# Optimization experiments

Hardware: AMD Instinct MI355X
Metric: run time of the kernel (lower is better)

## Reference

```python
import jax, jax.numpy as jnp
import numpy as np

Q, C, D, H, K, B, T = 10000, 200, 64, 64, 4, 512, 200
MAX_DISC = 10.0


def setup_inputs() -> dict:
    key = jax.random.key(0)
    ks = jax.random.split(key, 24)

    def p(k, shape, s=0.05):
        return jax.random.normal(k, shape, jnp.float32) * s

    mid_qd = (D + C) // 2   # 132
    mid_la = (H + C) // 2   # 132
    mid_dc = (D + 1) // 2   # 32
    inp = {
        'E_q': p(ks[0], (Q + 1, D)),
        'E_c': p(ks[1], (C + 1, D)),
        'E_it': p(ks[2], (101, D)),
        'E_ut': p(ks[3], (101, D)),
        'E_nh': p(ks[4], (101, D)),
        'W_fuse': p(ks[5], (D, 3 * D)), 'b_fuse': jnp.zeros((D,), jnp.float32),
        'W_ih': p(ks[6], (3 * H, 5 * D)), 'b_ih': jnp.zeros((3 * H,), jnp.float32),
        'W_hh': p(ks[7], (3 * H, H)), 'b_hh': jnp.zeros((3 * H,), jnp.float32),
        'qd_W1': p(ks[8], (mid_qd, D)), 'qd_b1': jnp.zeros((mid_qd,), jnp.float32),
        'qd_W2': p(ks[9], (C, mid_qd)), 'qd_b2': jnp.zeros((C,), jnp.float32),
        'la_W1': p(ks[10], (mid_la, H)), 'la_b1': jnp.zeros((mid_la,), jnp.float32),
        'la_W2': p(ks[11], (C, mid_la)), 'la_b2': jnp.zeros((C,), jnp.float32),
        'dc_W1': p(ks[12], (mid_dc, D)), 'dc_b1': jnp.zeros((mid_dc,), jnp.float32),
        'dc_W2': p(ks[13], (1, mid_dc)), 'dc_b2': jnp.zeros((1,), jnp.float32),
    }
    inp['question_seq'] = jax.random.randint(ks[14], (B, T), 0, Q + 1, jnp.int32)
    inp['correct_seq'] = jax.random.randint(ks[15], (B, T), 0, 2, jnp.int32)
    inp['interval_time_seq'] = jax.random.randint(ks[16], (B, T), 0, 101, jnp.int32)
    inp['use_time_seq'] = jax.random.randint(ks[17], (B, T), 0, 101, jnp.int32)
    inp['num_hint_seq'] = jax.random.randint(ks[18], (B, T), 0, 101, jnp.int32)
    inp['num_attempt_seq'] = jax.random.randint(ks[19], (B, T), 0, 101, jnp.int32)
    # per-question concept lists + padding mask (first nc entries valid)
    q2c = jax.random.randint(ks[20], (Q + 1, K), 0, C, jnp.int32)
    nc = jax.random.randint(ks[21], (Q + 1,), 1, K + 1, jnp.int32)
    mask = (jnp.arange(K, dtype=jnp.int32)[None, :] < nc[:, None]).astype(jnp.int32)
    inp['q2c_table'] = q2c
    inp['q2c_mask'] = mask
    rows = jnp.arange(Q + 1)[:, None]
    inp['Q_table'] = jnp.zeros((Q + 1, C), jnp.float32).at[rows, q2c].max(mask.astype(jnp.float32))
    return inp


def mlp2(x, W1, b1, W2, b2):
    # MLP4Proj, num_layer=2, eval-mode dropout == identity
    return jax.nn.relu(x @ W1.T + b1) @ W2.T + b2


def gru(x, W_ih, b_ih, W_hh, b_hh):
    # torch nn.GRU, 1 layer, batch_first; gate order r,z,n
    xp = jnp.einsum('btd,gd->btg', x, W_ih) + b_ih  # [B,T,3H]

    def step(h, xp_t):
        gh = h @ W_hh.T + b_hh
        xr, xz, xn = jnp.split(xp_t, 3, axis=-1)
        hr, hz, hn = jnp.split(gh, 3, axis=-1)
        r = jax.nn.sigmoid(xr + hr)
        z = jax.nn.sigmoid(xz + hz)
        n = jnp.tanh(xn + r * hn)
        h_new = (1.0 - z) * n + z * h
        return h_new, h_new

    h0 = jnp.zeros((x.shape[0], W_hh.shape[1]), x.dtype)
    _, hs = jax.lax.scan(step, h0, jnp.swapaxes(xp, 0, 1))
    return jnp.swapaxes(hs, 0, 1)  # [B,T,H]


def reference(E_q, E_c, E_it, E_ut, E_nh, W_fuse, b_fuse, W_ih, b_ih, W_hh, b_hh,
              qd_W1, qd_b1, qd_W2, qd_b2, la_W1, la_b1, la_W2, la_b2,
              dc_W1, dc_b1, dc_W2, dc_b2, Q_table,
              question_seq, correct_seq, interval_time_seq, use_time_seq,
              num_hint_seq, num_attempt_seq, q2c_table, q2c_mask):
    qe = E_q[question_seq]                                   # [B,T,D]
    # get_concept_emb: difficulty-weighted concept fusion
    qd = jax.nn.sigmoid(mlp2(qe, qd_W1, qd_b1, qd_W2, qd_b2))  # [B,T,C]
    qc_idx = q2c_table[question_seq]                          # [B,T,K]
    msk = q2c_mask[question_seq].astype(qe.dtype)             # [B,T,K]
    rel = jnp.take_along_axis(qd, qc_idx, axis=2) * msk       # [B,T,K]
    srel = rel.sum(-1, keepdims=True) + 1e-6
    ce = (rel[..., None] * E_c[qc_idx]).sum(-2) / srel        # [B,T,D]
    corr = jnp.broadcast_to(correct_seq[..., None].astype(qe.dtype), qe.shape)
    inter = jnp.concatenate([qe, ce, corr], axis=-1)          # [B,T,3D]
    # aux-info fusion (source bug: num_attempt also uses embed_num_hint)
    ut_nh_na = jnp.concatenate([E_ut[use_time_seq], E_nh[num_hint_seq], E_nh[num_attempt_seq]], axis=-1)
    fuse = ut_nh_na @ W_fuse.T + b_fuse                       # [B,T,D]
    x = jnp.concatenate([inter, E_it[interval_time_seq], fuse], axis=-1)  # [B,T,5D]
    latent = gru(x, W_ih, b_ih, W_hh, b_hh)                   # [B,T,H]
    # predict_score on shifted slices
    lat, qe2, qs2 = latent[:, :-1], qe[:, 1:], question_seq[:, 1:]
    ua = jax.nn.sigmoid(mlp2(lat, la_W1, la_b1, la_W2, la_b2))       # [B,T-1,C]
    disc = jax.nn.sigmoid(mlp2(qe2, dc_W1, dc_b1, dc_W2, dc_b2)) * MAX_DISC  # [B,T-1,1]
    qd2 = jax.nn.sigmoid(mlp2(qe2, qd_W1, qd_b1, qd_W2, qd_b2))      # [B,T-1,C]
    Qt = Q_table[qs2]                                                # [B,T-1,C]
    ua_m = ua * Qt
    qd_m = qd2 * Qt
    sw = qd_m.sum(-1, keepdims=True) + 1e-6
    y = disc * (ua_m - qd_m) / sw
    return jax.nn.sigmoid(y.sum(-1))                                 # [B,T-1]
```

## Files before the change

### kernel.cpp

```cpp
#include <hip/hip_runtime.h>
#include <hip/hip_fp16.h>

constexpr int QN  = 10001;
constexpr int BB  = 512;
constexpr int TT  = 200;
constexpr int QPB = 32;

__device__ __forceinline__ float sigm(float x) { return 1.f / (1.f + __expf(-x)); }
__device__ __forceinline__ float tanh_fast(float x) { return 1.f - 2.f / (1.f + __expf(2.f * x)); }

__device__ __forceinline__ unsigned packh_rtne(float lo, float hi) {
    return ((unsigned)__half_as_ushort(__float2half(hi)) << 16) |
            (unsigned)__half_as_ushort(__float2half(lo));
}

typedef _Float16 half2_t __attribute__((ext_vector_type(2)));
__device__ __forceinline__ half2_t u2h(unsigned u) {
    union { unsigned u; half2_t h; } x; x.u = u; return x.h;
}

#if __has_builtin(__builtin_amdgcn_fdot2)
__device__ __forceinline__ float fdot2u(unsigned wu, unsigned hu, float acc) {
    return __builtin_amdgcn_fdot2(u2h(wu), u2h(hu), acc, false);
}
#else
__device__ __forceinline__ float fdot2u(unsigned wu, unsigned hu, float acc) {
    float wlo = __half2float(__ushort_as_half((unsigned short)(wu & 0xffffu)));
    float whi = __half2float(__ushort_as_half((unsigned short)(wu >> 16)));
    float hlo = __half2float(__ushort_as_half((unsigned short)(hu & 0xffffu)));
    float hhi = __half2float(__ushort_as_half((unsigned short)(hu >> 16)));
    return acc + wlo * hlo + whi * hhi;
}
#endif

__global__ void k_tables(const float* __restrict__ E_c, const float* __restrict__ E_it,
                         const float* __restrict__ E_ut, const float* __restrict__ E_nh,
                         const float* __restrict__ W_fuse, const float* __restrict__ b_fuse,
                         const float* __restrict__ W_ih, const float* __restrict__ b_ih,
                         float* __restrict__ T_c, float* __restrict__ T_it,
                         float* __restrict__ T_ut, float* __restrict__ T_nh, float* __restrict__ T_na,
                         float* __restrict__ bias0, float* __restrict__ Vcorr)
{
    int blk = blockIdx.x, j = threadIdx.x;
    __shared__ float s_e[64];
    __shared__ float s_t[64];

    if (blk < 201) {
        if (j < 64) s_e[j] = E_c[blk * 64 + j];
        __syncthreads();
        float a = 0.f;
        #pragma unroll
        for (int k = 0; k < 64; k++) a += W_ih[j * 320 + 64 + k] * s_e[k];
        T_c[blk * 192 + j] = a;
    } else if (blk < 302) {
        int r = blk - 201;
        if (j < 64) s_e[j] = E_it[r * 64 + j];
        __syncthreads();
        float a = 0.f;
        #pragma unroll
        for (int k = 0; k < 64; k++) a += W_ih[j * 320 + 192 + k] * s_e[k];
        T_it[r * 192 + j] = a;
    } else if (blk < 605) {
        int which = (blk - 302) / 101;
        int r     = (blk - 302) % 101;
        const float* E = (which == 0) ? E_ut : E_nh;
        int fofs = which * 64;
        if (j < 64) s_e[j] = E[r * 64 + j];
        __syncthreads();
        if (j < 64) {
            float a = 0.f;
            #pragma unroll
            for (int d = 0; d < 64; d++) a += W_fuse[j * 192 + fofs + d] * s_e[d];
            s_t[j] = a;
        }
        __syncthreads();
        float a = 0.f;
        #pragma unroll
        for (int e = 0; e < 64; e++) a += W_ih[j * 320 + 256 + e] * s_t[e];
        float* outp = (which == 0) ? T_ut : ((which == 1) ? T_nh : T_na);
        outp[r * 192 + j] = a;
    } else {
        float a = b_ih[j];
        #pragma unroll
        for (int e = 0; e < 64; e++) a += W_ih[j * 320 + 256 + e] * b_fuse[e];
        bias0[j] = a;
        float v = 0.f;
        #pragma unroll
        for (int k = 0; k < 64; k++) v += W_ih[j * 320 + 128 + k];
        Vcorr[j] = v;
    }
}

__global__ void __launch_bounds__(192) k_perq(
    const float* __restrict__ E_q, const float* __restrict__ W_ih,
    const float* __restrict__ qd_W1, const float* __restrict__ qd_b1,
    const float* __restrict__ qd_W2, const float* __restrict__ qd_b2,
    const float* __restrict__ dc_W1, const float* __restrict__ dc_b1,
    const float* __restrict__ dc_W2, const float* __restrict__ dc_b2,
    const int* __restrict__ q2c, const int* __restrict__ q2cm,
    const float* __restrict__ T_c,
    float* __restrict__ Xq, float* __restrict__ disc,
    float* __restrict__ qds, float* __restrict__ wdk)
{
    __shared__ float s_wbuf[192 * 66];
    __shared__ float s_qe[QPB][64];
    __shared__ float s_wq[QPB][4];
    __shared__ int   s_cq[QPB][4];
    __shared__ float s_hidw[3][136];

    const int tid = threadIdx.x, w = tid >> 6, l = tid & 63;
    const int q0 = blockIdx.x * QPB;

    for (int i = tid; i < 132 * 64; i += 192)
        s_wbuf[(i >> 6) * 66 + (i & 63)] = qd_W1[i];
    for (int i = tid; i < 32 * 64; i += 192)
        s_wbuf[(132 + (i >> 6)) * 66 + (i & 63)] = dc_W1[i];
    for (int i = tid; i < QPB * 64; i += 192) {
        int qq = i >> 6, q = q0 + qq;
        s_qe[qq][i & 63] = E_q[(q < QN ? q : 0) * 64 + (i & 63)];
    }
    __syncthreads();

    for (int qq = w; qq < QPB; qq += 3) {
        int q = q0 + qq;
        bool valid = q < QN;
        int qc = valid ? q : 0;
        int cc[4], mm[4];
        #pragma unroll
        for (int k = 0; k < 4; k++) { cc[k] = q2c[qc * 4 + k]; mm[k] = q2cm[qc * 4 + k]; }

        float qe[64];
        #pragma unroll
        for (int k4 = 0; k4 < 16; k4++) {
            float4 v = *(const float4*)(&s_qe[qq][k4 * 4]);
            qe[4 * k4] = v.x; qe[4 * k4 + 1] = v.y; qe[4 * k4 + 2] = v.z; qe[4 * k4 + 3] = v.w;
        }

        auto rowdot = [&](int r) {
            const float* wr = s_wbuf + r * 66;
            float a = 0.f;
            #pragma unroll
            for (int jj = 0; jj < 32; jj++) {
                float2 ww = *(const float2*)(wr + 2 * jj);
                a += ww.x * qe[2 * jj] + ww.y * qe[2 * jj + 1];
            }
            return a;
        };

        s_hidw[w][l]      = fmaxf(rowdot(l)      + qd_b1[l],      0.f);
        s_hidw[w][64 + l] = fmaxf(rowdot(64 + l) + qd_b1[64 + l], 0.f);
        if (l < 4)
            s_hidw[w][128 + l] = fmaxf(rowdot(128 + l) + qd_b1[128 + l], 0.f);
        float dch = 0.f;
        if (l < 32) dch = fmaxf(rowdot(132 + l) + dc_b1[l], 0.f);

        int g = l >> 4, li = l & 15;
        int c = cc[g];
        float acc = 0.f;
        #pragma unroll
        for (int i = 0; i < 9; i++) {
            int m = li + 16 * i;
            if (m < 132) acc += qd_W2[c * 132 + m] * s_hidw[w][m];
        }
        acc += __shfl_xor(acc, 1); acc += __shfl_xor(acc, 2);
        acc += __shfl_xor(acc, 4); acc += __shfl_xor(acc, 8);
        float r0 = __shfl(acc, 0), r1 = __shfl(acc, 16);
        float r2 = __shfl(acc, 32), r3 = __shfl(acc, 48);

        float raw[4] = { sigm(r0 + qd_b2[cc[0]]), sigm(r1 + qd_b2[cc[1]]),
                         sigm(r2 + qd_b2[cc[2]]), sigm(r3 + qd_b2[cc[3]]) };
        float rel[4];
        #pragma unroll
        for (int k = 0; k < 4; k++) rel[k] = raw[k] * (float)mm[k];
        float sr = rel[0] + rel[1] + rel[2] + rel[3] + 1e-6f;

        float qsum = 0.f, wdv[4];
        #pragma unroll
        for (int k = 0; k < 4; k++) {
            float wd = 0.f;
            if (mm[k]) {
                bool dup = false;
                for (int jj = 0; jj < k; jj++)
                    if (mm[jj] && cc[jj] == cc[k]) dup = true;
                if (!dup) { wd = 1.f; qsum += raw[k]; }
            }
            wdv[k] = wd;
        }
        if (l < 4) { s_wq[qq][l] = rel[l] / sr; s_cq[qq][l] = cc[l]; }
        if (valid) {
            if (l < 4) wdk[q * 4 + l] = wdv[l];
            if (l == 0) qds[q] = qsum;
        }

        float dv = (l < 32) ? dch * dc_W2[l] : 0.f;
        dv += __shfl_xor(dv, 1);  dv += __shfl_xor(dv, 2);
        dv += __shfl_xor(dv, 4);  dv += __shfl_xor(dv, 8);
        dv += __shfl_xor(dv, 16);
        if (valid && l == 0) disc[q] = sigm(dv + dc_b2[0]) * 10.f;
    }

    __syncthreads();
    for (int i = tid; i < 192 * 64; i += 192) {
        int r = i >> 6, k = i & 63;
        s_wbuf[r * 66 + k] = W_ih[r * 320 + k];
    }
    __syncthreads();

    for (int qq = w; qq < QPB; qq += 3) {
        int q = q0 + qq;
        if (q >= QN) continue;

        float qe[64];
        #pragma unroll
        for (int k4 = 0; k4 < 16; k4++) {
            float4 v = *(const float4*)(&s_qe[qq][k4 * 4]);
            qe[4 * k4] = v.x; qe[4 * k4 + 1] = v.y; qe[4 * k4 + 2] = v.z; qe[4 * k4 + 3] = v.w;
        }
        float wq[4]; int cq[4];
        #pragma unroll
        for (int k = 0; k < 4; k++) { wq[k] = s_wq[qq][k]; cq[k] = s_cq[qq][k]; }

        #pragma unroll
        for (int rr = 0; rr < 3; rr++) {
            int row = rr * 64 + l;
            const float* wr = s_wbuf + row * 66;
            float a = 0.f;
            #pragma unroll
            for (int jj = 0; jj < 32; jj++) {
                float2 ww = *(const float2*)(wr + 2 * jj);
                a += ww.x * qe[2 * jj] + ww.y * qe[2 * jj + 1];
            }
            #pragma unroll
            for (int k = 0; k < 4; k++) a += wq[k] * T_c[cq[k] * 192 + row];
            Xq[q * 192 + row] = a;
        }
    }
}

__global__ void
__launch_bounds__(64)
__attribute__((amdgpu_waves_per_eu(1, 1)))
k_gru(
    const float* __restrict__ W_hh, const float* __restrict__ b_hh,
    const float* __restrict__ Xq, const float* __restrict__ Tit, const float* __restrict__ Tut,
    const float* __restrict__ Tnh, const float* __restrict__ Tna,
    const float* __restrict__ b0, const float* __restrict__ vc,
    const int* __restrict__ qseq, const int* __restrict__ cseq, const int* __restrict__ itseq,
    const int* __restrict__ utseq, const int* __restrict__ nhseq, const int* __restrict__ naseq,
    float* __restrict__ latent)
{
    const int j = threadIdx.x, b = blockIdx.x;

    __shared__ unsigned s_hp[32];
    __shared__ int s_ix[6 * TT];

    const int base = b * TT;
    for (int i = j; i < TT; i += 64) {
        s_ix[i]          = qseq[base + i];
        s_ix[TT + i]     = cseq[base + i];
        s_ix[2 * TT + i] = itseq[base + i];
        s_ix[3 * TT + i] = utseq[base + i];
        s_ix[4 * TT + i] = nhseq[base + i];
        s_ix[5 * TT + i] = naseq[base + i];
    }

    unsigned wr[32], wz[32], wn[32];
    {
        const float4* p0 = (const float4*)(W_hh + j * 64);
        const float4* p1 = (const float4*)(W_hh + (64 + j) * 64);
        const float4* p2 = (const float4*)(W_hh + (128 + j) * 64);
        #pragma unroll
        for (int k = 0; k < 16; k++) {
            float4 a = p0[k], bq = p1[k], c = p2[k];
            wr[2 * k] = packh_rtne(a.x, a.y);  wr[2 * k + 1] = packh_rtne(a.z, a.w);
            wz[2 * k] = packh_rtne(bq.x, bq.y); wz[2 * k + 1] = packh_rtne(bq.z, bq.w);
            wn[2 * k] = packh_rtne(c.x, c.y);  wn[2 * k + 1] = packh_rtne(c.z, c.w);
        }
    }
    #pragma unroll
    for (int k = 0; k < 32; k++)
        asm volatile("" : "+v"(wr[k]), "+v"(wz[k]), "+v"(wn[k]));

    const float bhr = b_hh[j], bhz = b_hh[64 + j], bhn = b_hh[128 + j];
    const float b0r = b0[j],   b0z = b0[64 + j],   b0n = b0[128 + j];
    const float vcr = vc[j],   vcz = vc[64 + j],   vcn = vc[128 + j];

    if (j < 32) s_hp[j] = 0u;
    float hj = 0.f;

    float A[15], B[15], C[15], D[15], cA, cB, cC, cD;

#define GATHER(G, CC, tt) { \
        int q_ = s_ix[tt], c_ = s_ix[TT + tt], it_ = s_ix[2 * TT + tt]; \
        int ut_ = s_ix[3 * TT + tt], nh_ = s_ix[4 * TT + tt], na_ = s_ix[5 * TT + tt]; \
        CC = (float)c_; \
        const float* xq_ = Xq  + q_  * 192 + j; \
        const float* ti_ = Tit + it_ * 192 + j; \
        const float* tu_ = Tut + ut_ * 192 + j; \
        const float* tn_ = Tnh + nh_ * 192 + j; \
        const float* ta_ = Tna + na_ * 192 + j; \
        G[0] = xq_[0]; G[1]  = xq_[64]; G[2]  = xq_[128]; \
        G[3] = ti_[0]; G[4]  = ti_[64]; G[5]  = ti_[128]; \
        G[6] = tu_[0]; G[7]  = tu_[64]; G[8]  = tu_[128]; \
        G[9] = tn_[0]; G[10] = tn_[64]; G[11] = tn_[128]; \
        G[12] = ta_[0]; G[13] = ta_[64]; G[14] = ta_[128]; \
    }

#define STEP(G, CC, tcur) { \
        float xr = b0r + CC * vcr + (((G[0] + G[3]) + (G[6] + G[9]))  + G[12]); \
        float xz = b0z + CC * vcz + (((G[1] + G[4]) + (G[7] + G[10])) + G[13]); \
        float xn = b0n + CC * vcn + (((G[2] + G[5]) + (G[8] + G[11])) + G[14]); \
        if ((tcur) + 4 < TT) GATHER(G, CC, (tcur) + 4); \
        float ar0 = 0.f, ar1 = 0.f, ar2 = 0.f, ar3 = 0.f; \
        float az0 = 0.f, az1 = 0.f, az2 = 0.f, az3 = 0.f; \
        float an0 = 0.f, an1 = 0.f, an2 = 0.f, an3 = 0.f; \
        const uint4* hp4 = (const uint4*)s_hp; \
        _Pragma("unroll") \
        for (int k4 = 0; k4 < 8; k4++) { \
            uint4 hh = hp4[k4]; \
            ar0 = fdot2u(wr[4 * k4 + 0], hh.x, ar0); \
            ar1 = fdot2u(wr[4 * k4 + 1], hh.y, ar1); \
            ar2 = fdot2u(wr[4 * k4 + 2], hh.z, ar2); \
            ar3 = fdot2u(wr[4 * k4 + 3], hh.w, ar3); \
            az0 = fdot2u(wz[4 * k4 + 0], hh.x, az0); \
            az1 = fdot2u(wz[4 * k4 + 1], hh.y, az1); \
            az2 = fdot2u(wz[4 * k4 + 2], hh.z, az2); \
            az3 = fdot2u(wz[4 * k4 + 3], hh.w, az3); \
            an0 = fdot2u(wn[4 * k4 + 0], hh.x, an0); \
            an1 = fdot2u(wn[4 * k4 + 1], hh.y, an1); \
            an2 = fdot2u(wn[4 * k4 + 2], hh.z, an2); \
            an3 = fdot2u(wn[4 * k4 + 3], hh.w, an3); \
        } \
        float ar = ((ar0 + ar1) + (ar2 + ar3)) + bhr; \
        float az = ((az0 + az1) + (az2 + az3)) + bhz; \
        float an = ((an0 + an1) + (an2 + an3)) + bhn; \
        float r = sigm(xr + ar); \
        float z = sigm(xz + az); \
        float n = tanh_fast(xn + r * an); \
        hj = (1.f - z) * n + z * hj; \
        latent[(size_t)(base + (tcur)) * 64 + j] = hj; \
        float hnb = __shfl_xor(hj, 1); \
        unsigned pk = (j & 1) ? packh_rtne(hnb, hj) : packh_rtne(hj, hnb); \
        if (!(j & 1)) s_hp[j >> 1] = pk; \
    }

    GATHER(A, cA, 0);
    GATHER(B, cB, 1);
    GATHER(C, cC, 2);
    GATHER(D, cD, 3);

    for (int t = 0; t < TT; t += 4) {
        STEP(A, cA, t);
        STEP(B, cB, t + 1);
        STEP(C, cC, t + 2);
        STEP(D, cD, t + 3);
    }
#undef STEP
#undef GATHER
}

__global__ void __launch_bounds__(256) k_final(
    const float* __restrict__ latent, const int* __restrict__ qseq,
    const float* __restrict__ la_W1, const float* __restrict__ la_b1,
    const float* __restrict__ la_W2, const float* __restrict__ la_b2,
    const int* __restrict__ q2c,
    const float* __restrict__ disc, const float* __restrict__ qds,
    const float* __restrict__ wdk, float* __restrict__ out)
{
    __shared__ unsigned short s_w2[200 * 132];
    __shared__ float s_b2[200];

    const int tid = threadIdx.x;
    for (int i = tid; i < 200 * 132; i += 256)
        s_w2[i] = __half_as_ushort(__float2half(la_W2[i]));
    for (int i = tid; i < 200; i += 256) s_b2[i] = la_b2[i];
    __syncthreads();

    int o = blockIdx.x * blockDim.x + tid;
    if (o >= BB * (TT - 1)) return;
    int b = o / (TT - 1), t = o - b * (TT - 1);

    const float* lat = latent + (size_t)(b * TT + t) * 64;
    float l[64];
    #pragma unroll
    for (int k4 = 0; k4 < 16; k4++) {
        float4 v = ((const float4*)lat)[k4];
        l[k4 * 4] = v.x; l[k4 * 4 + 1] = v.y; l[k4 * 4 + 2] = v.z; l[k4 * 4 + 3] = v.w;
    }

    int q = qseq[b * TT + t + 1];
    int c0 = q2c[q * 4], c1 = q2c[q * 4 + 1], c2 = q2c[q * 4 + 2], c3 = q2c[q * 4 + 3];
    const unsigned short* w0p = s_w2 + c0 * 132;
    const unsigned short* w1p = s_w2 + c1 * 132;
    const unsigned short* w2p = s_w2 + c2 * 132;
    const unsigned short* w3p = s_w2 + c3 * 132;

    float u0 = 0.f, u1 = 0.f, u2 = 0.f, u3 = 0.f;
    for (int m = 0; m < 132; m++) {
        float a = la_b1[m];
        const float* w = la_W1 + m * 64;
        #pragma unroll
        for (int k = 0; k < 64; k++) a += w[k] * l[k];
        float hm = fmaxf(a, 0.f);
        u0 += __half2float(__ushort_as_half(w0p[m])) * hm;
        u1 += __half2float(__ushort_as_half(w1p[m])) * hm;
        u2 += __half2float(__ushort_as_half(w2p[m])) * hm;
        u3 += __half2float(__ushort_as_half(w3p[m])) * hm;
    }

    float w0 = wdk[q * 4], w1 = wdk[q * 4 + 1], w2 = wdk[q * 4 + 2], w3 = wdk[q * 4 + 3];
    float us = w0 * sigm(u0 + s_b2[c0]) + w1 * sigm(u1 + s_b2[c1])
             + w2 * sigm(u2 + s_b2[c2]) + w3 * sigm(u3 + s_b2[c3]);
    float qs = qds[q];
    float y = disc[q] * (us - qs) / (qs + 1e-6f);
    out[o] = sigm(y);
}

extern "C" void kernel_launch(void* const* d_in, const int* in_sizes, int n_in,
                              void* d_out, int out_size, void* d_ws, size_t ws_size,
                              hipStream_t stream)
{
    const float* E_q    = (const float*)d_in[0];
    const float* E_c    = (const float*)d_in[1];
    const float* E_it   = (const float*)d_in[2];
    const float* E_ut   = (const float*)d_in[3];
    const float* E_nh   = (const float*)d_in[4];
    const float* W_fuse = (const float*)d_in[5];
    const float* b_fuse = (const float*)d_in[6];
    const float* W_ih   = (const float*)d_in[7];
    const float* b_ih   = (const float*)d_in[8];
    const float* W_hh   = (const float*)d_in[9];
    const float* b_hh   = (const float*)d_in[10];
    const float* qd_W1  = (const float*)d_in[11];
    const float* qd_b1  = (const float*)d_in[12];
    const float* qd_W2  = (const float*)d_in[13];
    const float* qd_b2  = (const float*)d_in[14];
    const float* la_W1  = (const float*)d_in[15];
    const float* la_b1  = (const float*)d_in[16];
    const float* la_W2  = (const float*)d_in[17];
    const float* la_b2  = (const float*)d_in[18];
    const float* dc_W1  = (const float*)d_in[19];
    const float* dc_b1  = (const float*)d_in[20];
    const float* dc_W2  = (const float*)d_in[21];
    const float* dc_b2  = (const float*)d_in[22];

    int off = (in_sizes[23] == QN * 200) ? 1 : 0;
    const int* qseq  = (const int*)d_in[23 + off];
    const int* cseq  = (const int*)d_in[24 + off];
    const int* itseq = (const int*)d_in[25 + off];
    const int* utseq = (const int*)d_in[26 + off];
    const int* nhseq = (const int*)d_in[27 + off];
    const int* naseq = (const int*)d_in[28 + off];
    const int* q2c   = (const int*)d_in[29 + off];
    const int* q2cm  = (const int*)d_in[30 + off];

    float* ws = (float*)d_ws;
    size_t o = 0;
    float* T_c  = ws + o; o += (size_t)201 * 192;
    float* Tit  = ws + o; o += (size_t)101 * 192;
    float* Tut  = ws + o; o += (size_t)101 * 192;
    float* Tnh  = ws + o; o += (size_t)101 * 192;
    float* Tna  = ws + o; o += (size_t)101 * 192;
    float* b0   = ws + o; o += 192;
    float* vc   = ws + o; o += 192;
    float* Xq   = ws + o; o += (size_t)QN * 192;
    float* disc = ws + o; o += QN;
    float* qds  = ws + o; o += QN;
    float* wdk  = ws + o; o += (size_t)QN * 4;
    float* latent = ws + o; o += (size_t)BB * TT * 64;

    float* outp = (float*)d_out;

    k_tables<<<606, 192, 0, stream>>>(E_c, E_it, E_ut, E_nh, W_fuse, b_fuse, W_ih, b_ih,
                                      T_c, Tit, Tut, Tnh, Tna, b0, vc);
    k_perq<<<(QN + QPB - 1) / QPB, 192, 0, stream>>>(E_q, W_ih, qd_W1, qd_b1, qd_W2, qd_b2,
                                                     dc_W1, dc_b1, dc_W2, dc_b2, q2c, q2cm, T_c,
                                                     Xq, disc, qds, wdk);
    k_gru<<<BB, 64, 0, stream>>>(W_hh, b_hh, Xq, Tit, Tut, Tnh, Tna, b0, vc,
                                 qseq, cseq, itseq, utseq, nhseq, naseq, latent);
    k_final<<<(BB * (TT - 1) + 255) / 256, 256, 0, stream>>>(latent, qseq, la_W1, la_b1,
                                                             la_W2, la_b2, q2c, disc, qds, wdk, outp);
}
```

Measured before the change: 335.8 us.

## Interleave GRU gate tables and gather them with vector dwordx4 loads

The per-question and per-feature input-gate tables are rewritten in an interleaved layout, so each hidden unit's r/z/n values sit next to each other. The GRU kernel then fetches them with one global_load_dwordx4 per table instead of three scalar loads. This cuts the gather from fifteen loads to five per timestep in the latency-bound recurrence. Prefetch waits are handled with explicit s_waitcnt vmcnt counts in inline asm. The cost is one over-read element per load, covered by padding, and hand-managed counters that can stall more than needed because stores also count against vmcnt.

```diff
diff --git a/kernel.cpp b/kernel.cpp
--- a/kernel.cpp
+++ b/kernel.cpp
@@ -15,6 +15,7 @@
 }
 
 typedef _Float16 half2_t __attribute__((ext_vector_type(2)));
+typedef float f4v __attribute__((ext_vector_type(4)));
 __device__ __forceinline__ half2_t u2h(unsigned u) {
     union { unsigned u; half2_t h; } x; x.u = u; return x.h;
 }
@@ -44,6 +45,7 @@
     int blk = blockIdx.x, j = threadIdx.x;
     __shared__ float s_e[64];
     __shared__ float s_t[64];
+    const int ilv = (j & 63) * 3 + (j >> 6);
 
     if (blk < 201) {
         if (j < 64) s_e[j] = E_c[blk * 64 + j];
@@ -59,7 +61,7 @@
         float a = 0.f;
         #pragma unroll
         for (int k = 0; k < 64; k++) a += W_ih[j * 320 + 192 + k] * s_e[k];
-        T_it[r * 192 + j] = a;
+        T_it[r * 192 + ilv] = a;
     } else if (blk < 605) {
         int which = (blk - 302) / 101;
         int r     = (blk - 302) % 101;
@@ -78,7 +80,7 @@
         #pragma unroll
         for (int e = 0; e < 64; e++) a += W_ih[j * 320 + 256 + e] * s_t[e];
         float* outp = (which == 0) ? T_ut : ((which == 1) ? T_nh : T_na);
-        outp[r * 192 + j] = a;
+        outp[r * 192 + ilv] = a;
     } else {
         float a = b_ih[j];
         #pragma unroll
@@ -232,7 +234,7 @@
             }
             #pragma unroll
             for (int k = 0; k < 4; k++) a += wq[k] * T_c[cq[k] * 192 + row];
-            Xq[q * 192 + row] = a;
+            Xq[q * 192 + l * 3 + rr] = a;
         }
     }
 }
@@ -242,14 +244,15 @@
 __attribute__((amdgpu_waves_per_eu(1, 1)))
 k_gru(
     const float* __restrict__ W_hh, const float* __restrict__ b_hh,
-    const float* __restrict__ Xq, const float* __restrict__ Tit, const float* __restrict__ Tut,
-    const float* __restrict__ Tnh, const float* __restrict__ Tna,
+    const float* __restrict__ XqI, const float* __restrict__ TitI, const float* __restrict__ TutI,
+    const float* __restrict__ TnhI, const float* __restrict__ TnaI,
     const float* __restrict__ b0, const float* __restrict__ vc,
     const int* __restrict__ qseq, const int* __restrict__ cseq, const int* __restrict__ itseq,
     const int* __restrict__ utseq, const int* __restrict__ nhseq, const int* __restrict__ naseq,
     float* __restrict__ latent)
 {
     const int j = threadIdx.x, b = blockIdx.x;
+    const int j3 = 3 * j;
 
     __shared__ unsigned s_hp[32];
     __shared__ int s_ix[6 * TT];
@@ -288,29 +291,29 @@
     if (j < 32) s_hp[j] = 0u;
     float hj = 0.f;
 
-    float A[15], B[15], C[15], D[15], cA, cB, cC, cD;
-
-#define GATHER(G, CC, tt) { \
+    f4v A0, A1, A2, A3, A4;  float cA;
+    f4v B0, B1, B2, B3, B4;  float cB;
+    f4v C0, C1, C2, C3, C4;  float cC;
+    f4v D0, D1, D2, D3, D4;  float cD;
+
+#define GISSUE(P, CC, tt) { \
         int q_ = s_ix[tt], c_ = s_ix[TT + tt], it_ = s_ix[2 * TT + tt]; \
         int ut_ = s_ix[3 * TT + tt], nh_ = s_ix[4 * TT + tt], na_ = s_ix[5 * TT + tt]; \
         CC = (float)c_; \
-        const float* xq_ = Xq  + q_  * 192 + j; \
-        const float* ti_ = Tit + it_ * 192 + j; \
-        const float* tu_ = Tut + ut_ * 192 + j; \
-        const float* tn_ = Tnh + nh_ * 192 + j; \
-        const float* ta_ = Tna + na_ * 192 + j; \
-        G[0] = xq_[0]; G[1]  = xq_[64]; G[2]  = xq_[128]; \
-        G[3] = ti_[0]; G[4]  = ti_[64]; G[5]  = ti_[128]; \
-        G[6] = tu_[0]; G[7]  = tu_[64]; G[8]  = tu_[128]; \
-        G[9] = tn_[0]; G[10] = tn_[64]; G[11] = tn_[128]; \
-        G[12] = ta_[0]; G[13] = ta_[64]; G[14] = ta_[128]; \
-    }
-
-#define STEP(G, CC, tcur) { \
-        float xr = b0r + CC * vcr + (((G[0] + G[3]) + (G[6] + G[9]))  + G[12]); \
-        float xz = b0z + CC * vcz + (((G[1] + G[4]) + (G[7] + G[10])) + G[13]); \
-        float xn = b0n + CC * vcn + (((G[2] + G[5]) + (G[8] + G[11])) + G[14]); \
-        if ((tcur) + 4 < TT) GATHER(G, CC, (tcur) + 4); \
+        asm volatile("global_load_dwordx4 %0, %1, off" : "=v"(P##0) : "v"(XqI  + q_  * 192 + j3)); \
+        asm volatile("global_load_dwordx4 %0, %1, off" : "=v"(P##1) : "v"(TitI + it_ * 192 + j3)); \
+        asm volatile("global_load_dwordx4 %0, %1, off" : "=v"(P##2) : "v"(TutI + ut_ * 192 + j3)); \
+        asm volatile("global_load_dwordx4 %0, %1, off" : "=v"(P##3) : "v"(TnhI + nh_ * 192 + j3)); \
+        asm volatile("global_load_dwordx4 %0, %1, off" : "=v"(P##4) : "v"(TnaI + na_ * 192 + j3)); \
+    }
+
+#define STEP(P, CC, tcur, WN, REF) { \
+        asm volatile("s_waitcnt vmcnt(" WN ")" ::: "memory"); \
+        float xr = b0r + CC * vcr + ((((P##0).x + (P##1).x) + ((P##2).x + (P##3).x)) + (P##4).x); \
+        float xz = b0z + CC * vcz + ((((P##0).y + (P##1).y) + ((P##2).y + (P##3).y)) + (P##4).y); \
+        float xn = b0n + CC * vcn + ((((P##0).z + (P##1).z) + ((P##2).z + (P##3).z)) + (P##4).z); \
+        asm volatile("" :: "v"((P##0).w), "v"((P##1).w), "v"((P##2).w), "v"((P##3).w), "v"((P##4).w)); \
+        if (REF) GISSUE(P, CC, (tcur) + 4); \
         float ar0 = 0.f, ar1 = 0.f, ar2 = 0.f, ar3 = 0.f; \
         float az0 = 0.f, az1 = 0.f, az2 = 0.f, az3 = 0.f; \
         float an0 = 0.f, an1 = 0.f, an2 = 0.f, an3 = 0.f; \
@@ -344,19 +347,23 @@
         if (!(j & 1)) s_hp[j >> 1] = pk; \
     }
 
-    GATHER(A, cA, 0);
-    GATHER(B, cB, 1);
-    GATHER(C, cC, 2);
-    GATHER(D, cD, 3);
-
-    for (int t = 0; t < TT; t += 4) {
-        STEP(A, cA, t);
-        STEP(B, cB, t + 1);
-        STEP(C, cC, t + 2);
-        STEP(D, cD, t + 3);
-    }
+    GISSUE(A, cA, 0);
+    GISSUE(B, cB, 1);
+    GISSUE(C, cC, 2);
+    GISSUE(D, cD, 3);
+
+    for (int t = 0; t < TT - 4; t += 4) {
+        STEP(A, cA, t,     "15", 1);
+        STEP(B, cB, t + 1, "15", 1);
+        STEP(C, cC, t + 2, "15", 1);
+        STEP(D, cD, t + 3, "15", 1);
+    }
+    STEP(A, cA, TT - 4, "15", 0);
+    STEP(B, cB, TT - 3, "10", 0);
+    STEP(C, cC, TT - 2, "5",  0);
+    STEP(D, cD, TT - 1, "0",  0);
 #undef STEP
-#undef GATHER
+#undef GISSUE
 }
 
 __global__ void __launch_bounds__(256) k_final(
@@ -456,14 +463,14 @@
 
     float* ws = (float*)d_ws;
     size_t o = 0;
-    float* T_c  = ws + o; o += (size_t)201 * 192;
-    float* Tit  = ws + o; o += (size_t)101 * 192;
-    float* Tut  = ws + o; o += (size_t)101 * 192;
-    float* Tnh  = ws + o; o += (size_t)101 * 192;
-    float* Tna  = ws + o; o += (size_t)101 * 192;
+    float* T_c  = ws + o; o += (size_t)201 * 192 + 4;
+    float* Tit  = ws + o; o += (size_t)101 * 192 + 4;
+    float* Tut  = ws + o; o += (size_t)101 * 192 + 4;
+    float* Tnh  = ws + o; o += (size_t)101 * 192 + 4;
+    float* Tna  = ws + o; o += (size_t)101 * 192 + 4;
     float* b0   = ws + o; o += 192;
     float* vc   = ws + o; o += 192;
-    float* Xq   = ws + o; o += (size_t)QN * 192;
+    float* Xq   = ws + o; o += (size_t)QN * 192 + 4;
     float* disc = ws + o; o += QN;
     float* qds  = ws + o; o += QN;
     float* wdk  = ws + o; o += (size_t)QN * 4;
```

After: 324.6 us. 3.3% less time.
